# Optimization experiments

Measured on AMD Instinct MI355X. Metric: run time of the kernel, lower is better.

Reference implementation:

```python
import jax, jax.numpy as jnp
import numpy as np

B, S, N, D = 1, 512, 384, 64
H, DP, DQK = 32, 128, 64
LAMBDA_INIT = 1.0
EPS = 1e-32
SCALING = DQK ** -0.5


def _layer_norm(x, g, b):
    m = jnp.mean(x, axis=-1, keepdims=True)
    v = jnp.mean(jnp.square(x - m), axis=-1, keepdims=True)
    return (x - m) * jax.lax.rsqrt(v + 1e-5) * g + b


def setup_inputs() -> dict:
    key = jax.random.key(0)
    ks = jax.random.split(key, 12)
    msa = jax.random.normal(ks[0], (B, S, N, D), dtype=jnp.float32)
    Wq = jax.random.normal(ks[1], (2 * DQK, D), dtype=jnp.float32) * 0.02
    Wk = Wq + jax.random.normal(ks[2], (2 * DQK, D), dtype=jnp.float32) * 0.1 * 0.02
    Wl = jax.random.normal(ks[3], (H, D), dtype=jnp.float32) * 0.02
    Wr = jax.random.normal(ks[4], (H, D), dtype=jnp.float32) * 0.02
    Wp = jax.random.normal(ks[5], (2 * DP, H * H), dtype=jnp.float32) * 0.02
    bp = jnp.zeros((2 * DP,), dtype=jnp.float32)
    lq1 = jax.random.normal(ks[6], (DQK,), dtype=jnp.float32) * 0.1
    lk1 = jax.random.normal(ks[7], (DQK,), dtype=jnp.float32) * 0.1
    lq2 = jax.random.normal(ks[8], (DQK,), dtype=jnp.float32) * 0.1
    lk2 = jax.random.normal(ks[9], (DQK,), dtype=jnp.float32) * 0.1
    return {
        'msa': msa,
        'ln_g': jnp.ones((D,), jnp.float32), 'ln_b': jnp.zeros((D,), jnp.float32),
        'Wq': Wq, 'Wk': Wk,
        'qn_g': jnp.ones((DQK,), jnp.float32), 'qn_b': jnp.zeros((DQK,), jnp.float32),
        'kn_g': jnp.ones((DQK,), jnp.float32), 'kn_b': jnp.zeros((DQK,), jnp.float32),
        'lq1': lq1, 'lk1': lk1, 'lq2': lq2, 'lk2': lk2,
        'Wl': Wl, 'Wr': Wr, 'Wp': Wp, 'bp': bp,
    }


def reference(msa, ln_g, ln_b, Wq, Wk, qn_g, qn_b, kn_g, kn_b,
              lq1, lk1, lq2, lk2, Wl, Wr, Wp, bp):
    b, s, n, d = msa.shape
    x = _layer_norm(msa, ln_g, ln_b)  # [b,s,n,d]

    # differential sequence attention (all masks are all-True by default)
    q = (x[:, 0] @ Wq.T).reshape(b, n, 2, DQK).transpose(0, 2, 1, 3)       # [b,2,n,dqk]
    k = (x @ Wk.T).reshape(b, s, n, 2, DQK).transpose(0, 3, 1, 2, 4)       # [b,2,s,n,dqk]
    q = _layer_norm(q, qn_g, qn_b)
    k = _layer_norm(k, kn_g, kn_b)
    sw = jnp.einsum('btnd,btsnd->btsn', q, k) * SCALING                     # [b,2,s,n]
    sw = sw.sum(axis=-1) / (n + EPS)                                        # [b,2,s]
    lam = jnp.exp(jnp.sum(lq1 * lk1)) - jnp.exp(jnp.sum(lq2 * lk2)) + LAMBDA_INIT
    sw = sw[:, 0] - lam * sw[:, 1]                                          # [b,s]
    seq_weights = jax.nn.softmax(sw, axis=-1)                               # [b,s]

    # weighted left/right hidden projections
    a = jnp.einsum('bsnd,hd->bnsh', x, Wl)
    bt = jnp.einsum('bsnd,hd->bnsh', x, Wr)
    ws = jnp.sqrt(seq_weights + EPS)[:, None, :, None]                      # [b,1,s,1]
    a = a * ws
    bt = bt * ws

    # outer product mean over sequences, then pairwise projection + SwiGLU
    outer = jnp.einsum('bisc,bjse->bijce', a, bt).reshape(b, n, n, H * H)   # [b,n,n,h^2]
    out = outer @ Wp.T + bp                                                 # [b,n,n,2*dp]
    val, gate = jnp.split(out, 2, axis=-1)
    return jax.nn.silu(gate) * val                                          # [b,n,n,dp]
```

## Files before the change

### kernel.cpp

```cpp
#include <hip/hip_runtime.h>
#include <hip/hip_bf16.h>
#include <math.h>

#define WS_X        0u
#define WS_AEXT     12582912u
#define WS_BEXT     18874368u
#define WS_QG       25165824u
#define WS_SQG      25214976u
#define WS_SQB      25215744u
#define WS_PART     25216512u
#define WS_WSQ      25219584u
#define WS_BPP      25220096u
#define WS_WPF      25220352u

typedef __attribute__((ext_vector_type(8))) short bf16x8;
typedef __attribute__((ext_vector_type(4))) float f32x4;

union U4B8 { uint4 u4; unsigned u[4]; bf16x8 v; };

__device__ __forceinline__ unsigned short f2b(float x) {
    __hip_bfloat16 b = __float2bfloat16(x);
    return *reinterpret_cast<unsigned short*>(&b);
}
__device__ __forceinline__ float b2f(unsigned short u) {
    __hip_bfloat16 b = *reinterpret_cast<__hip_bfloat16*>(&u);
    return __bfloat162float(b);
}

#define GLDS(g, l) __builtin_amdgcn_global_load_lds(                                   \
    (const __attribute__((address_space(1))) unsigned int*)(g),                        \
    (__attribute__((address_space(3))) unsigned int*)(l), 16, 0, 0)

#define MFMA16(a, b, c) __builtin_amdgcn_mfma_f32_16x16x32_bf16((a), (b), (c), 0, 0, 0)

__global__ __launch_bounds__(256) void k1_ln(const float* __restrict__ msa,
                                             const float* __restrict__ g,
                                             const float* __restrict__ bb,
                                             float* __restrict__ x) {
    int row = blockIdx.x * 16 + (threadIdx.x >> 4);
    int l16 = threadIdx.x & 15;
    float4 v = ((const float4*)msa)[(size_t)row * 16 + l16];
    float sum = v.x + v.y + v.z + v.w;
    #pragma unroll
    for (int m = 1; m < 16; m <<= 1) sum += __shfl_xor(sum, m);
    float mean = sum * (1.0f / 64.0f);
    float4 dv = make_float4(v.x - mean, v.y - mean, v.z - mean, v.w - mean);
    float sq = dv.x * dv.x + dv.y * dv.y + dv.z * dv.z + dv.w * dv.w;
    #pragma unroll
    for (int m = 1; m < 16; m <<= 1) sq += __shfl_xor(sq, m);
    float r = rsqrtf(sq * (1.0f / 64.0f) + 1e-5f);
    float4 g4 = ((const float4*)g)[l16];
    float4 b4 = ((const float4*)bb)[l16];
    ((float4*)x)[(size_t)row * 16 + l16] = make_float4(
        dv.x * r * g4.x + b4.x, dv.y * r * g4.y + b4.y,
        dv.z * r * g4.z + b4.z, dv.w * r * g4.w + b4.w);
}

__global__ __launch_bounds__(128) void k2_q(const float* __restrict__ x,
                                            const float* __restrict__ Wq,
                                            const float* __restrict__ qg_,
                                            const float* __restrict__ qb_,
                                            const float* __restrict__ kg_,
                                            const float* __restrict__ kb_,
                                            float* __restrict__ qgOut,
                                            float* __restrict__ SqgOut,
                                            float* __restrict__ SqbOut) {
    int n = blockIdx.x;
    int tt = threadIdx.x >> 6;
    int d = threadIdx.x & 63;
    const float* xr = x + (size_t)n * 64;
    const float* w  = Wq + (size_t)(tt * 64 + d) * 64;
    float acc = 0.f;
    #pragma unroll 8
    for (int dd = 0; dd < 64; ++dd) acc += xr[dd] * w[dd];
    float sum = acc;
    #pragma unroll
    for (int m = 1; m < 64; m <<= 1) sum += __shfl_xor(sum, m);
    float mean = sum * (1.0f / 64.0f);
    float dv = acc - mean;
    float sq = dv * dv;
    #pragma unroll
    for (int m = 1; m < 64; m <<= 1) sq += __shfl_xor(sq, m);
    float r = rsqrtf(sq * (1.0f / 64.0f) + 1e-5f);
    float qnv = dv * r * qg_[d] + qb_[d];
    float qgv = qnv * kg_[d];
    float sb  = qnv * kb_[d];
    float sg  = qgv;
    #pragma unroll
    for (int m = 1; m < 64; m <<= 1) { sg += __shfl_xor(sg, m); sb += __shfl_xor(sb, m); }
    qgOut[(size_t)(tt * 384 + n) * 64 + d] = qgv;
    if (d == 0) { SqgOut[tt * 384 + n] = sg; SqbOut[tt * 384 + n] = sb; }
}

__global__ __launch_bounds__(256) void gemm_k3(const float* __restrict__ X,
                                               const float* __restrict__ Wk,
                                               const float* __restrict__ qg,
                                               const float* __restrict__ Sqg,
                                               const float* __restrict__ Sqb,
                                               float* __restrict__ part) {
    __shared__ __align__(16) char smem[65536];
    float (*AsT)[132] = (float(*)[132])smem;
    float (*BsT)[132] = (float(*)[132])(smem + 16896);
    float* kbuf = (float*)smem;

    int t  = threadIdx.x;
    int m0 = blockIdx.x * 128;
    int s  = m0 / 384;
    int nchunk = (m0 - s * 384) >> 7;
    int tr = t >> 4, tc = t & 15;
    float acc[8][8] = {};
    int rrow = t >> 3;
    int kk   = (t & 7) * 4;
    for (int k0 = 0; k0 < 64; k0 += 32) {
        #pragma unroll
        for (int l = 0; l < 4; ++l) {
            int row = rrow + 32 * l;
            float4 va = *(const float4*)(X + (size_t)(m0 + row) * 64 + k0 + kk);
            AsT[kk + 0][row] = va.x; AsT[kk + 1][row] = va.y;
            AsT[kk + 2][row] = va.z; AsT[kk + 3][row] = va.w;
            float4 vb = *(const float4*)(Wk + (size_t)row * 64 + k0 + kk);
            BsT[kk + 0][row] = vb.x; BsT[kk + 1][row] = vb.y;
            BsT[kk + 2][row] = vb.z; BsT[kk + 3][row] = vb.w;
        }
        __syncthreads();
        #pragma unroll 4
        for (int k = 0; k < 32; ++k) {
            float a[8], b[8];
            *(float4*)&a[0] = *(const float4*)&AsT[k][tr * 8];
            *(float4*)&a[4] = *(const float4*)&AsT[k][tr * 8 + 4];
            *(float4*)&b[0] = *(const float4*)&BsT[k][tc * 8];
            *(float4*)&b[4] = *(const float4*)&BsT[k][tc * 8 + 4];
            #pragma unroll
            for (int q = 0; q < 8; ++q)
                #pragma unroll
                for (int j = 0; j < 8; ++j)
                    acc[q][j] += a[q] * b[j];
        }
        __syncthreads();
    }
    #pragma unroll
    for (int q = 0; q < 8; ++q) {
        int m = tr * 8 + q;
        int swz = (m & 15) << 4;
        int b0 = m * 512 + (((tc * 2) * 16) ^ swz);
        int b1 = m * 512 + (((tc * 2 + 1) * 16) ^ swz);
        *(float4*)((char*)kbuf + b0) = make_float4(acc[q][0], acc[q][1], acc[q][2], acc[q][3]);
        *(float4*)((char*)kbuf + b1) = make_float4(acc[q][4], acc[q][5], acc[q][6], acc[q][7]);
    }
    __syncthreads();
    int r  = t & 127;
    int tt = t >> 7;
    int n  = nchunk * 128 + r;
    const char* base = (const char*)kbuf + r * 512;
    const float4* qgp = (const float4*)(qg + ((size_t)(tt * 384 + n)) * 64);
    int swz = (r & 15) << 4;
    float s1 = 0.f, s2 = 0.f, s3 = 0.f;
    #pragma unroll
    for (int i = 0; i < 16; ++i) {
        float4 kv = *(const float4*)(base + ((((tt * 16 + i) * 16) ^ swz)));
        float4 qv = qgp[i];
        s1 += kv.x + kv.y + kv.z + kv.w;
        s2 += kv.x * kv.x + kv.y * kv.y + kv.z * kv.z + kv.w * kv.w;
        s3 += kv.x * qv.x + kv.y * qv.y + kv.z * qv.z + kv.w * qv.w;
    }
    float mu  = s1 * (1.0f / 64.0f);
    float var = s2 * (1.0f / 64.0f) - mu * mu;
    float rln = rsqrtf(var + 1e-5f);
    float dot = rln * (s3 - mu * Sqg[tt * 384 + n]) + Sqb[tt * 384 + n];
    #pragma unroll
    for (int m = 1; m < 64; m <<= 1) dot += __shfl_xor(dot, m);
    __syncthreads();
    if ((t & 63) == 0) kbuf[t >> 6] = dot;
    __syncthreads();
    if (t == 0) part[((size_t)0 * 512 + s) * 3 + nchunk] = kbuf[0] + kbuf[1];
    if (t == 1) part[((size_t)1 * 512 + s) * 3 + nchunk] = kbuf[2] + kbuf[3];
}

__global__ __launch_bounds__(512) void k4_softmax(const float* __restrict__ part,
                                                  const float* __restrict__ lq1,
                                                  const float* __restrict__ lk1,
                                                  const float* __restrict__ lq2,
                                                  const float* __restrict__ lk2,
                                                  float* __restrict__ wsq) {
    int s = threadIdx.x;
    float l1 = 0.f, l2 = 0.f;
    for (int i = 0; i < 64; ++i) { l1 += lq1[i] * lk1[i]; l2 += lq2[i] * lk2[i]; }
    float lam = expf(l1) - expf(l2) + 1.0f;
    const float c = 0.125f / 384.0f;
    float a0 = (part[s * 3] + part[s * 3 + 1] + part[s * 3 + 2]) * c;
    float a1 = (part[(512 + s) * 3] + part[(512 + s) * 3 + 1] + part[(512 + s) * 3 + 2]) * c;
    float v = a0 - lam * a1;
    __shared__ float red[512];
    red[s] = v;
    __syncthreads();
    for (int off = 256; off > 0; off >>= 1) {
        if (s < off) red[s] = fmaxf(red[s], red[s + off]);
        __syncthreads();
    }
    float mx = red[0];
    __syncthreads();
    float e = expf(v - mx);
    red[s] = e;
    __syncthreads();
    for (int off = 256; off > 0; off >>= 1) {
        if (s < off) red[s] += red[s + off];
        __syncthreads();
    }
    wsq[s] = sqrtf(e / red[0] + 1e-32f);
}

__global__ __launch_bounds__(256) void k5_ab(const float* __restrict__ x,
                                             const float* __restrict__ Wl,
                                             const float* __restrict__ Wr,
                                             const float* __restrict__ wsq,
                                             unsigned short* __restrict__ AHo,
                                             unsigned short* __restrict__ ALo,
                                             unsigned short* __restrict__ BHo,
                                             unsigned short* __restrict__ BLo) {
    int i  = blockIdx.x;
    int s0 = blockIdx.y * 64;
    int t  = threadIdx.x;
    __shared__ __align__(16) float wl[2048], wr[2048];
    __shared__ float xT[64][69];
    ((float4*)wl)[t * 2]     = ((const float4*)Wl)[t * 2];
    ((float4*)wl)[t * 2 + 1] = ((const float4*)Wl)[t * 2 + 1];
    ((float4*)wr)[t * 2]     = ((const float4*)Wr)[t * 2];
    ((float4*)wr)[t * 2 + 1] = ((const float4*)Wr)[t * 2 + 1];
    {
        int s_l = t >> 2, d0 = (t & 3) * 16;
        const float* xr = x + ((size_t)(s0 + s_l) * 384 + i) * 64 + d0;
        #pragma unroll
        for (int j = 0; j < 4; ++j) {
            float4 v = *(const float4*)(xr + j * 4);
            xT[d0 + j * 4 + 0][s_l] = v.x; xT[d0 + j * 4 + 1][s_l] = v.y;
            xT[d0 + j * 4 + 2][s_l] = v.z; xT[d0 + j * 4 + 3][s_l] = v.w;
        }
    }
    __syncthreads();
    int c = t >> 3, so = (t & 7) * 8;
    float aa[8] = {}, bb2[8] = {};
    #pragma unroll 8
    for (int d = 0; d < 64; ++d) {
        float wlv = wl[c * 64 + d], wrv = wr[c * 64 + d];
        #pragma unroll
        for (int q = 0; q < 8; ++q) {
            float xv = xT[d][so + q];
            aa[q]  += xv * wlv;
            bb2[q] += xv * wrv;
        }
    }
    #pragma unroll
    for (int q = 0; q < 8; ++q) {
        float wq = wsq[s0 + so + q];
        aa[q] *= wq; bb2[q] *= wq;
    }
    int m = i * 32 + c;
    int s = s0 + so;
    size_t idx = (((size_t)(m >> 4) * 16 + (s >> 5)) * 64 + ((m & 15) | (((s >> 3) & 3) << 4))) * 8;
    {
        unsigned short h[8], l[8];
        #pragma unroll
        for (int q = 0; q < 8; ++q) { h[q] = f2b(aa[q]); l[q] = f2b(aa[q] - b2f(h[q])); }
        *(uint4*)&AHo[idx] = make_uint4((unsigned)h[0] | ((unsigned)h[1] << 16), (unsigned)h[2] | ((unsigned)h[3] << 16),
                                        (unsigned)h[4] | ((unsigned)h[5] << 16), (unsigned)h[6] | ((unsigned)h[7] << 16));
        *(uint4*)&ALo[idx] = make_uint4((unsigned)l[0] | ((unsigned)l[1] << 16), (unsigned)l[2] | ((unsigned)l[3] << 16),
                                        (unsigned)l[4] | ((unsigned)l[5] << 16), (unsigned)l[6] | ((unsigned)l[7] << 16));
    }
    {
        unsigned short h[8], l[8];
        #pragma unroll
        for (int q = 0; q < 8; ++q) { h[q] = f2b(bb2[q]); l[q] = f2b(bb2[q] - b2f(h[q])); }
        *(uint4*)&BHo[idx] = make_uint4((unsigned)h[0] | ((unsigned)h[1] << 16), (unsigned)h[2] | ((unsigned)h[3] << 16),
                                        (unsigned)h[4] | ((unsigned)h[5] << 16), (unsigned)h[6] | ((unsigned)h[7] << 16));
        *(uint4*)&BLo[idx] = make_uint4((unsigned)l[0] | ((unsigned)l[1] << 16), (unsigned)l[2] | ((unsigned)l[3] << 16),
                                        (unsigned)l[4] | ((unsigned)l[5] << 16), (unsigned)l[6] | ((unsigned)l[7] << 16));
    }
}

__global__ __launch_bounds__(256) void prep_wp(const float* __restrict__ Wp,
                                               const float* __restrict__ bp,
                                               unsigned short* __restrict__ WpF,
                                               float* __restrict__ bpP) {
    int gid = blockIdx.x * 256 + threadIdx.x;
    int lane  = gid & 63;
    int kstep = (gid >> 6) & 31;
    int nb    = (gid >> 11) & 15;
    int bsel  = gid >> 15;
    int rl = lane & 15, kg = lane >> 4;
    int urow = nb * 16 + rl;
    int srow = (urow & 1) ? 128 + (urow >> 1) : (urow >> 1);
    int k0 = kstep * 32 + kg * 8;
    const float* src = Wp + (size_t)srow * 1024 + k0;
    unsigned short o[8];
    #pragma unroll
    for (int e = 0; e < 8; ++e) {
        float w = src[e];
        unsigned short h = f2b(w);
        o[e] = bsel ? f2b(w - b2f(h)) : h;
    }
    *(uint4*)&WpF[(size_t)gid * 8] = make_uint4(
        (unsigned)o[0] | ((unsigned)o[1] << 16), (unsigned)o[2] | ((unsigned)o[3] << 16),
        (unsigned)o[4] | ((unsigned)o[5] << 16), (unsigned)o[6] | ((unsigned)o[7] << 16));
    if (blockIdx.x == 0) {
        int tt = threadIdx.x;
        bpP[tt] = bp[(tt & 1) ? 128 + (tt >> 1) : (tt >> 1)];
    }
}

__global__ __launch_bounds__(256, 3) void gemm_fused(const unsigned short* __restrict__ AH,
                                                     const unsigned short* __restrict__ AL,
                                                     const unsigned short* __restrict__ BHm,
                                                     const unsigned short* __restrict__ BLm,
                                                     const unsigned short* __restrict__ WpF,
                                                     const float* __restrict__ bpP,
                                                     float* __restrict__ out) {
    __shared__ __align__(16) unsigned char smem[32768];
    unsigned* pa = (unsigned*)smem;

    const int t = threadIdx.x;
    const int wave = t >> 6, lane = t & 63;
    const int bx = blockIdx.x, by = blockIdx.y;
    const int m0 = bx * 128, n0 = by * 128;
    const int wm = (wave & 1) * 64, wn = (wave >> 1) * 64;
    const int kgrp = lane >> 4, rl = lane & 15;
    f32x4 acc[4][4] = {};

    const unsigned short* aHb = AH + (size_t)((m0 + wm) >> 4) * 8192 + lane * 8;
    const unsigned short* aLb = AL + (size_t)((m0 + wm) >> 4) * 8192 + lane * 8;
    const unsigned short* bArr = (wave < 2) ? BHm : BLm;
    const unsigned short* bSrc = bArr + (size_t)((n0 >> 4) + (wave & 1) * 4) * 8192 + lane * 8;
    const int dstOffB = (wave >> 1) * 8192 + (wave & 1) * 4096;

    bf16x8 aHr[4], aLr[4];
    #pragma unroll
    for (int p = 0; p < 4; ++p)
        GLDS(bSrc + (size_t)p * 8192, (unsigned short*)(smem + dstOffB + p * 1024));
    #pragma unroll
    for (int f = 0; f < 4; ++f) {
        aHr[f] = *(const bf16x8*)(aHb + (size_t)f * 8192);
        aLr[f] = *(const bf16x8*)(aLb + (size_t)f * 8192);
    }
    __syncthreads();

    #pragma unroll 2
    for (int kt = 0; kt < 16; ++kt) {
        const int cur = kt & 1, nxt = cur ^ 1;
        if (kt < 15) {
            const unsigned short* s2 = bSrc + (size_t)(kt + 1) * 512;
            #pragma unroll
            for (int p = 0; p < 4; ++p)
                GLDS(s2 + (size_t)p * 8192, (unsigned short*)(smem + nxt * 16384 + dstOffB + p * 1024));
        }
        const int cb = cur * 16384;
        __builtin_amdgcn_s_setprio(1);
        #pragma unroll
        for (int nf = 0; nf < 4; ++nf) {
            const int pB = ((wn >> 4) + nf) * 1024;
            bf16x8 bHf = *(const bf16x8*)(smem + cb + pB + lane * 16);
            bf16x8 bLf = *(const bf16x8*)(smem + cb + 8192 + pB + lane * 16);
            #pragma unroll
            for (int mf = 0; mf < 4; ++mf) {
                acc[mf][nf] = MFMA16(aHr[mf], bHf, acc[mf][nf]);
                acc[mf][nf] = MFMA16(aLr[mf], bHf, acc[mf][nf]);
                acc[mf][nf] = MFMA16(aHr[mf], bLf, acc[mf][nf]);
            }
        }
        __builtin_amdgcn_s_setprio(0);
        if (kt < 15) {
            #pragma unroll
            for (int f = 0; f < 4; ++f) {
                aHr[f] = *(const bf16x8*)(aHb + (size_t)f * 8192 + (kt + 1) * 512);
                aLr[f] = *(const bf16x8*)(aLb + (size_t)f * 8192 + (kt + 1) * 512);
            }
        }
        __syncthreads();
    }

    f32x4 acc2[4] = {};
    const int kg8 = kgrp * 8;
    #pragma unroll
    for (int h = 0; h < 2; ++h) {
        #pragma unroll
        for (int mi = 0; mi < 2; ++mi) {
            const int mf = mi * 2 + h;
            #pragma unroll
            for (int nf = 0; nf < 4; ++nf) {
                #pragma unroll
                for (int r = 0; r < 4; ++r) {
                    int mloc = wm + mf * 16 + kgrp * 4 + r;
                    int nloc = wn + nf * 16 + rl;
                    int p  = ((mloc >> 5) << 2) | (nloc >> 5);
                    int kl = ((mloc & 15) << 5) | (nloc & 31);
                    float v = acc[mf][nf][r];
                    unsigned short hh = f2b(v);
                    unsigned short ll = f2b(v - b2f(hh));
                    pa[(p << 9) + (kl ^ ((p & 3) << 3))] = (unsigned)hh | ((unsigned)ll << 16);
                }
            }
        }
        __syncthreads();
        const unsigned* paRow = pa + (rl << 9);
        #pragma unroll 4
        for (int ksl = 0; ksl < 16; ++ksl) {
            const int ks = h * 16 + ksl;
            U4B8 ua0, ua1, aHf, aLf;
            int kb = (ksl * 32 + kg8) ^ ((rl & 3) << 3);
            ua0.u4 = *(const uint4*)(paRow + kb);
            ua1.u4 = *(const uint4*)(paRow + kb + 4);
            aHf.u[0] = __builtin_amdgcn_perm(ua0.u[1], ua0.u[0], 0x05040100u);
            aHf.u[1] = __builtin_amdgcn_perm(ua0.u[3], ua0.u[2], 0x05040100u);
            aHf.u[2] = __builtin_amdgcn_perm(ua1.u[1], ua1.u[0], 0x05040100u);
            aHf.u[3] = __builtin_amdgcn_perm(ua1.u[3], ua1.u[2], 0x05040100u);
            aLf.u[0] = __builtin_amdgcn_perm(ua0.u[1], ua0.u[0], 0x07060302u);
            aLf.u[1] = __builtin_amdgcn_perm(ua0.u[3], ua0.u[2], 0x07060302u);
            aLf.u[2] = __builtin_amdgcn_perm(ua1.u[1], ua1.u[0], 0x07060302u);
            aLf.u[3] = __builtin_amdgcn_perm(ua1.u[3], ua1.u[2], 0x07060302u);
            #pragma unroll
            for (int nf = 0; nf < 4; ++nf) {
                const int nb = wave * 4 + nf;
                bf16x8 bHf = *(const bf16x8*)&WpF[(size_t)((nb * 32 + ks) * 64 + lane) * 8];
                bf16x8 bLf = *(const bf16x8*)&WpF[(size_t)(((16 + nb) * 32 + ks) * 64 + lane) * 8];
                acc2[nf] = MFMA16(aHf.v, bHf, acc2[nf]);
                acc2[nf] = MFMA16(aLf.v, bHf, acc2[nf]);
                acc2[nf] = MFMA16(aHf.v, bLf, acc2[nf]);
            }
        }
        __syncthreads();
    }

    const int parity = rl & 1;
    #pragma unroll
    for (int nf = 0; nf < 4; ++nf) {
        const int np = wave * 64 + nf * 16 + rl;
        const float bias = bpP[np];
        const int ocol = np >> 1;
        #pragma unroll
        for (int r = 0; r < 4; ++r) {
            float own = acc2[nf][r] + bias;
            float oth = __shfl_xor(own, 1);
            float v = parity ? oth : own;
            float g = parity ? own : oth;
            float res = v * (g / (1.0f + expf(-g)));
            if (parity == (r >> 1)) {
                int p = kgrp * 4 + r;
                int i = bx * 4 + (p >> 2);
                int j = by * 4 + (p & 3);
                out[((size_t)i * 384 + j) * 128 + ocol] = res;
            }
        }
    }
}

extern "C" void kernel_launch(void* const* d_in, const int* in_sizes, int n_in,
                              void* d_out, int out_size, void* d_ws, size_t ws_size,
                              hipStream_t stream) {
    const float* msa  = (const float*)d_in[0];
    const float* ln_g = (const float*)d_in[1];
    const float* ln_b = (const float*)d_in[2];
    const float* Wq   = (const float*)d_in[3];
    const float* Wk   = (const float*)d_in[4];
    const float* qn_g = (const float*)d_in[5];
    const float* qn_b = (const float*)d_in[6];
    const float* kn_g = (const float*)d_in[7];
    const float* kn_b = (const float*)d_in[8];
    const float* lq1  = (const float*)d_in[9];
    const float* lk1  = (const float*)d_in[10];
    const float* lq2  = (const float*)d_in[11];
    const float* lk2  = (const float*)d_in[12];
    const float* Wl   = (const float*)d_in[13];
    const float* Wr   = (const float*)d_in[14];
    const float* Wp   = (const float*)d_in[15];
    const float* bp   = (const float*)d_in[16];
    float* out = (float*)d_out;
    float* ws  = (float*)d_ws;

    float* x = ws + WS_X;
    unsigned short* AHs = (unsigned short*)(ws + WS_AEXT);
    unsigned short* ALs = (unsigned short*)(ws + WS_AEXT + 3145728u);
    unsigned short* BHs = (unsigned short*)(ws + WS_BEXT);
    unsigned short* BLs = (unsigned short*)(ws + WS_BEXT + 3145728u);
    float* qg   = ws + WS_QG;
    float* Sqg  = ws + WS_SQG;
    float* Sqb  = ws + WS_SQB;
    float* part = ws + WS_PART;
    float* wsq  = ws + WS_WSQ;
    float* bpP  = ws + WS_BPP;
    unsigned short* WpF = (unsigned short*)(ws + WS_WPF);

    prep_wp<<<256, 256, 0, stream>>>(Wp, bp, WpF, bpP);
    k1_ln<<<12288, 256, 0, stream>>>(msa, ln_g, ln_b, x);
    k2_q<<<384, 128, 0, stream>>>(x, Wq, qn_g, qn_b, kn_g, kn_b, qg, Sqg, Sqb);
    gemm_k3<<<1536, 256, 0, stream>>>(x, Wk, qg, Sqg, Sqb, part);
    k4_softmax<<<1, 512, 0, stream>>>(part, lq1, lk1, lq2, lk2, wsq);
    k5_ab<<<dim3(384, 8), 256, 0, stream>>>(x, Wl, Wr, wsq, AHs, ALs, BHs, BLs);
    gemm_fused<<<dim3(96, 96), 256, 0, stream>>>(AHs, ALs, BHs, BLs, WpF, bpP, out);
}
```

Baseline: 863.1 us.

## Triple-buffer B tiles and double-buffer A registers in fused GEMM main loop

Moves the fused GEMM main loop from LDS double buffering to a three-stage ring, issuing global-to-LDS loads two K-steps ahead. The A fragments for the next step are prefetched into a second register set before the current step's MFMAs. Loads are interleaved between per-fragment MFMA groups with raw s_barrier and a manual vmcnt wait, so memory latency is better hidden behind compute. In exchange, LDS grows to 48KB, the A registers double, and the occupancy hint of 3 blocks is dropped, which may lower occupancy. The extra barriers and hand-tuned waitcnt add risk of sync overhead or ordering bugs.

```diff
diff --git a/kernel.cpp b/kernel.cpp
--- a/kernel.cpp
+++ b/kernel.cpp
@@ -307,14 +307,14 @@
     }
 }
 
-__global__ __launch_bounds__(256, 3) void gemm_fused(const unsigned short* __restrict__ AH,
-                                                     const unsigned short* __restrict__ AL,
-                                                     const unsigned short* __restrict__ BHm,
-                                                     const unsigned short* __restrict__ BLm,
-                                                     const unsigned short* __restrict__ WpF,
-                                                     const float* __restrict__ bpP,
-                                                     float* __restrict__ out) {
-    __shared__ __align__(16) unsigned char smem[32768];
+__global__ __launch_bounds__(256) void gemm_fused(const unsigned short* __restrict__ AH,
+                                                  const unsigned short* __restrict__ AL,
+                                                  const unsigned short* __restrict__ BHm,
+                                                  const unsigned short* __restrict__ BLm,
+                                                  const unsigned short* __restrict__ WpF,
+                                                  const float* __restrict__ bpP,
+                                                  float* __restrict__ out) {
+    __shared__ __align__(16) unsigned char smem[49152];
     unsigned* pa = (unsigned*)smem;
 
     const int t = threadIdx.x;
@@ -331,50 +331,65 @@
     const unsigned short* bSrc = bArr + (size_t)((n0 >> 4) + (wave & 1) * 4) * 8192 + lane * 8;
     const int dstOffB = (wave >> 1) * 8192 + (wave & 1) * 4096;
 
-    bf16x8 aHr[4], aLr[4];
-    #pragma unroll
-    for (int p = 0; p < 4; ++p)
-        GLDS(bSrc + (size_t)p * 8192, (unsigned short*)(smem + dstOffB + p * 1024));
+    bf16x8 aHr[2][4], aLr[2][4];
     #pragma unroll
     for (int f = 0; f < 4; ++f) {
-        aHr[f] = *(const bf16x8*)(aHb + (size_t)f * 8192);
-        aLr[f] = *(const bf16x8*)(aLb + (size_t)f * 8192);
-    }
-    __syncthreads();
-
+        aHr[0][f] = *(const bf16x8*)(aHb + (size_t)f * 8192);
+        aLr[0][f] = *(const bf16x8*)(aLb + (size_t)f * 8192);
+    }
+    #pragma unroll
+    for (int p = 0; p < 4; ++p) {
+        GLDS(bSrc + (size_t)p * 8192,       (unsigned short*)(smem + dstOffB + p * 1024));
+        GLDS(bSrc + (size_t)p * 8192 + 512, (unsigned short*)(smem + 16384 + dstOffB + p * 1024));
+    }
+    __syncthreads();
+
+    int curB = 0, stageB = 2;
     #pragma unroll 2
     for (int kt = 0; kt < 16; ++kt) {
         const int cur = kt & 1, nxt = cur ^ 1;
-        if (kt < 15) {
-            const unsigned short* s2 = bSrc + (size_t)(kt + 1) * 512;
-            #pragma unroll
-            for (int p = 0; p < 4; ++p)
-                GLDS(s2 + (size_t)p * 8192, (unsigned short*)(smem + nxt * 16384 + dstOffB + p * 1024));
-        }
-        const int cb = cur * 16384;
-        __builtin_amdgcn_s_setprio(1);
-        #pragma unroll
-        for (int nf = 0; nf < 4; ++nf) {
-            const int pB = ((wn >> 4) + nf) * 1024;
-            bf16x8 bHf = *(const bf16x8*)(smem + cb + pB + lane * 16);
-            bf16x8 bLf = *(const bf16x8*)(smem + cb + 8192 + pB + lane * 16);
+        const unsigned char* bufc = smem + curB * 16384;
+        #pragma unroll
+        for (int p = 0; p < 4; ++p) {
+            const int pB = ((wn >> 4) + p) * 1024;
+            bf16x8 bHf = *(const bf16x8*)(bufc + pB + lane * 16);
+            bf16x8 bLf = *(const bf16x8*)(bufc + 8192 + pB + lane * 16);
+            if (p == 0 && kt < 15) {
+                #pragma unroll
+                for (int f = 0; f < 4; ++f) {
+                    aHr[nxt][f] = *(const bf16x8*)(aHb + (size_t)f * 8192 + (size_t)(kt + 1) * 512);
+                    aLr[nxt][f] = *(const bf16x8*)(aLb + (size_t)f * 8192 + (size_t)(kt + 1) * 512);
+                }
+            }
+            if (p == 2 && kt < 14) {
+                const unsigned short* s2 = bSrc + (size_t)(kt + 2) * 512;
+                unsigned char* dst = smem + stageB * 16384 + dstOffB;
+                #pragma unroll
+                for (int pp = 0; pp < 4; ++pp)
+                    GLDS(s2 + (size_t)pp * 8192, (unsigned short*)(dst + pp * 1024));
+            }
+            asm volatile("" ::: "memory");
+            __builtin_amdgcn_s_barrier();
+            asm volatile("" ::: "memory");
+            __builtin_amdgcn_s_setprio(1);
             #pragma unroll
             for (int mf = 0; mf < 4; ++mf) {
-                acc[mf][nf] = MFMA16(aHr[mf], bHf, acc[mf][nf]);
-                acc[mf][nf] = MFMA16(aLr[mf], bHf, acc[mf][nf]);
-                acc[mf][nf] = MFMA16(aHr[mf], bLf, acc[mf][nf]);
+                acc[mf][p] = MFMA16(aHr[cur][mf], bHf, acc[mf][p]);
+                acc[mf][p] = MFMA16(aLr[cur][mf], bHf, acc[mf][p]);
+                acc[mf][p] = MFMA16(aHr[cur][mf], bLf, acc[mf][p]);
             }
-        }
-        __builtin_amdgcn_s_setprio(0);
-        if (kt < 15) {
-            #pragma unroll
-            for (int f = 0; f < 4; ++f) {
-                aHr[f] = *(const bf16x8*)(aHb + (size_t)f * 8192 + (kt + 1) * 512);
-                aLr[f] = *(const bf16x8*)(aLb + (size_t)f * 8192 + (kt + 1) * 512);
-            }
-        }
-        __syncthreads();
-    }
+            __builtin_amdgcn_s_setprio(0);
+            asm volatile("" ::: "memory");
+            __builtin_amdgcn_s_barrier();
+            asm volatile("" ::: "memory");
+        }
+        asm volatile("s_waitcnt vmcnt(8)" ::: "memory");
+        __builtin_amdgcn_s_barrier();
+        asm volatile("" ::: "memory");
+        curB   = (curB == 2)   ? 0 : curB + 1;
+        stageB = (stageB == 2) ? 0 : stageB + 1;
+    }
+    __syncthreads();
 
     f32x4 acc2[4] = {};
     const int kg8 = kgrp * 8;
```

New measurement: 1.306 ms. 51.3% more time.
